# Kernel optimization log

Measured on AMD Instinct MI355X. Metric: run time of the kernel, lower is better.

The kernel has to match this reference:

```python
import jax, jax.numpy as jnp
from jax import lax
import numpy as np

THRESH = 0.5
R = 4  # suppression radius -> (2R+1)^3 max-pool window


def setup_inputs() -> dict:
    key = jax.random.key(0)
    pred_vol = jax.random.uniform(key, (1, 1, 64, 512, 512), dtype=jnp.float32)
    return {"pred_vol": pred_vol}


def reference(pred_vol):
    # Threshold: keep values above thresh, zero otherwise
    pred_thresh = jnp.where(pred_vol > THRESH, pred_vol, jnp.float32(0.0))
    # 3D max-pool, kernel 2R+1, stride 1, padding R (pad with -inf so padding
    k = 2 * R + 1
    conf = lax.reduce_window(
        pred_thresh,
        -jnp.inf,
        lax.max,
        window_dimensions=(1, 1, k, k, k),
        window_strides=(1, 1, 1, 1, 1),
        padding=[(0, 0), (0, 0), (R, R), (R, R), (R, R)],
    )
    # Keep only strict local maxima of the thresholded volume
    conf = jnp.where((conf > 0.0) & (conf == pred_thresh), conf, jnp.float32(0.0))
    return jnp.squeeze(conf)  # [D, H, W]
```

## Files before the change

### kernel.cpp

```cpp
#include <hip/hip_runtime.h>

static constexpr int Dd = 64;
static constexpr int Hh = 512;
static constexpr int Ww = 512;
static constexpr int RAD = 4;
static constexpr float THRESH_V = 0.5f;
static constexpr int W4 = Ww / 4;
static constexpr int PLANE4 = Hh * W4;

static constexpr int TH = 8;
static constexpr int DC = 16;
static constexpr int ROWS = TH + 2 * RAD;
static constexpr int NPL = DC + 2 * RAD;
static constexpr int NBLK = (Hh / TH) * (Dd / DC);

typedef float nf4 __attribute__((ext_vector_type(4)));

__device__ __forceinline__ float4 f4max(float4 a, float4 b) {
    return make_float4(fmaxf(a.x, b.x), fmaxf(a.y, b.y), fmaxf(a.z, b.z), fmaxf(a.w, b.w));
}
__device__ __forceinline__ int iclamp(int v, int lo, int hi) {
    return v < lo ? lo : (v > hi ? hi : v);
}

#define BAR_VM(N) asm volatile("s_waitcnt vmcnt(" #N ") lgkmcnt(0)\n\ts_barrier" ::: "memory")
#define BAR_LDS() asm volatile("s_waitcnt lgkmcnt(0)\n\ts_barrier" ::: "memory")

__device__ __forceinline__ void load_lds16(const float4* g, float4* l) {
    __builtin_amdgcn_global_load_lds(
        (const __attribute__((address_space(1))) void*)g,
        (__attribute__((address_space(3))) void*)l, 16, 0, 0);
}

__global__ __launch_bounds__(512, 1)
void fused_nms_k6(const float4* __restrict__ x4, float4* __restrict__ o4) {
    __shared__ float4 braw[3][ROWS * W4];
    __shared__ float4 bcol[TH * W4];

    const int tid  = threadIdx.x;
    const int w4   = tid & (W4 - 1);
    const int hs   = tid >> 7;
    const int wid  = tid >> 6;
    const int lane = tid & 63;

    const int b    = blockIdx.x;
    const int band = b & 7;
    const int rest = b >> 3;
    const int ht   = band * 8 + (rest & 7);
    const int dc   = rest >> 3;
    const int h0   = ht * TH;
    const int d0   = dc * DC;

    const int colm = w4 ? w4 - 1 : 0;
    const int colp = (w4 < W4 - 1) ? w4 + 1 : W4 - 1;

    int goff[4], loff[4];
#pragma unroll
    for (int k = 0; k < 4; ++k) {
        const int s    = wid + 8 * k;
        const int row  = s >> 1;
        const int half = s & 1;
        const int gh   = iclamp(h0 - RAD + row, 0, Hh - 1);
        goff[k] = gh * W4 + half * 64 + lane;
        loff[k] = row * W4 + half * 64;
    }

    auto stage = [&](int p) {
        const int gd = iclamp(d0 - RAD + p, 0, Dd - 1);
        const float4* pl = x4 + (size_t)gd * PLANE4;
        float4* dst = braw[p % 3];
#pragma unroll
        for (int k = 0; k < 4; ++k)
            load_lds16(pl + goff[k], dst + loff[k]);
    };

    auto hwin = [&](const float4 lm, const float4 cm, const float4 rm) -> float4 {
        const float l3 = lm.w, l2 = fmaxf(lm.z, l3), l1 = fmaxf(lm.y, l2), l0 = fmaxf(lm.x, l1);
        const float core = fmaxf(fmaxf(cm.x, cm.y), fmaxf(cm.z, cm.w));
        const float q0 = rm.x, q1 = fmaxf(q0, rm.y), q2 = fmaxf(q1, rm.z), q3 = fmaxf(q2, rm.w);
        float4 pm;
        pm.x = fmaxf(l0, fmaxf(core, q0));
        pm.y = fmaxf(l1, fmaxf(core, q1));
        pm.z = fmaxf(l2, fmaxf(core, q2));
        pm.w = fmaxf(l3, fmaxf(core, q3));
        return pm;
    };

    float4 R0[8], R1[8];
    float4 C0[4], C1[4];

    stage(0);
    stage(1);

#pragma unroll
    for (int t = 0; t < NPL; ++t) {
        const bool doE = (t >= 8);

        if (t <= 8)       { BAR_VM(4); }
        else if (t == 9)  { BAR_VM(6); }
        else if (t <= 22) { BAR_VM(8); }
        else              { BAR_VM(4); }

        if (t + 2 < NPL) stage(t + 2);
        __builtin_amdgcn_sched_barrier(0);

        const float4* Bc = &braw[t % 3][(2 * hs) * W4 + w4];
        float4 r0 = Bc[0 * W4], r1 = Bc[1 * W4], r2 = Bc[2 * W4], r3 = Bc[3 * W4];
        float4 r4 = Bc[4 * W4], r5 = Bc[5 * W4], r6 = Bc[6 * W4], r7 = Bc[7 * W4];
        float4 r8 = Bc[8 * W4], r9 = Bc[9 * W4];
        float4 core = f4max(f4max(f4max(r1, r2), f4max(r3, r4)),
                            f4max(f4max(r5, r6), f4max(r7, r8)));
        float4 v0 = f4max(core, r0);
        float4 v1 = f4max(core, r9);
        bcol[(2 * hs) * W4 + w4]     = v0;
        bcol[(2 * hs + 1) * W4 + w4] = v1;
        BAR_LDS();

        const float4 pm0 = hwin(bcol[(2 * hs) * W4 + colm],     v0, bcol[(2 * hs) * W4 + colp]);
        const float4 pm1 = hwin(bcol[(2 * hs + 1) * W4 + colm], v1, bcol[(2 * hs + 1) * W4 + colp]);

        if (doE) {
            const float4 cen0 = C0[t & 3];
            const float4 cen1 = C1[t & 3];
            float4 mm0 = pm0, mm1 = pm1;
#pragma unroll
            for (int i = 0; i < 8; ++i) { mm0 = f4max(mm0, R0[i]); mm1 = f4max(mm1, R1[i]); }
            const size_t obase = (size_t)(d0 + t - 8) * PLANE4 + (size_t)(h0 + 2 * hs) * W4 + w4;
            nf4 q0, q1;
            q0.x = (cen0.x > THRESH_V && cen0.x == mm0.x) ? cen0.x : 0.0f;
            q0.y = (cen0.y > THRESH_V && cen0.y == mm0.y) ? cen0.y : 0.0f;
            q0.z = (cen0.z > THRESH_V && cen0.z == mm0.z) ? cen0.z : 0.0f;
            q0.w = (cen0.w > THRESH_V && cen0.w == mm0.w) ? cen0.w : 0.0f;
            q1.x = (cen1.x > THRESH_V && cen1.x == mm1.x) ? cen1.x : 0.0f;
            q1.y = (cen1.y > THRESH_V && cen1.y == mm1.y) ? cen1.y : 0.0f;
            q1.z = (cen1.z > THRESH_V && cen1.z == mm1.z) ? cen1.z : 0.0f;
            q1.w = (cen1.w > THRESH_V && cen1.w == mm1.w) ? cen1.w : 0.0f;
            __builtin_nontemporal_store(q0, (nf4*)&o4[obase]);
            __builtin_nontemporal_store(q1, (nf4*)&o4[obase + W4]);
        }
        R0[t & 7] = pm0;  R1[t & 7] = pm1;
        C0[t & 3] = r4;   C1[t & 3] = r5;
    }
}

extern "C" void kernel_launch(void* const* d_in, const int* in_sizes, int n_in,
                              void* d_out, int out_size, void* d_ws, size_t ws_size,
                              hipStream_t stream) {
    const float4* x4 = (const float4*)d_in[0];
    float4* out4 = (float4*)d_out;
    (void)d_ws; (void)ws_size; (void)in_sizes; (void)n_in; (void)out_size;
    fused_nms_k6<<<dim3(NBLK), dim3(512), 0, stream>>>(x4, out4);
}
```

Before: 118.9 us.

## Software-pipeline vertical and horizontal max passes with double-buffered LDS

Double-buffers the column-max LDS buffer and skews the loop by one iteration, so the horizontal window for plane t-1 is computed in the same iteration as the vertical max for plane t. This removes one LDS barrier per plane between writing bcol and reading neighbours. The cost is one extra loop iteration, a larger center-value ring (5 entries), more registers and more LDS.

```diff
diff --git a/kernel.cpp b/kernel.cpp
--- a/kernel.cpp
+++ b/kernel.cpp
@@ -33,9 +33,9 @@
 }
 
 __global__ __launch_bounds__(512, 1)
-void fused_nms_k6(const float4* __restrict__ x4, float4* __restrict__ o4) {
+void fused_nms_k7(const float4* __restrict__ x4, float4* __restrict__ o4) {
     __shared__ float4 braw[3][ROWS * W4];
-    __shared__ float4 bcol[TH * W4];
+    __shared__ float4 bcol[2][TH * W4];
 
     const int tid  = threadIdx.x;
     const int w4   = tid & (W4 - 1);
@@ -87,59 +87,76 @@
     };
 
     float4 R0[8], R1[8];
-    float4 C0[4], C1[4];
+    float4 C0[5], C1[5];
+    float4 vp0, vp1;
 
     stage(0);
     stage(1);
 
 #pragma unroll
-    for (int t = 0; t < NPL; ++t) {
-        const bool doE = (t >= 8);
+    for (int t = 0; t <= NPL; ++t) {
+        const bool doV = (t <= NPL - 1);
+        const bool doH = (t >= 1);
+        const bool doE = (t >= 9);
 
-        if (t <= 8)       { BAR_VM(4); }
-        else if (t == 9)  { BAR_VM(6); }
+        if (t <= 9)       { BAR_VM(4); }
+        else if (t == 10) { BAR_VM(6); }
         else if (t <= 22) { BAR_VM(8); }
-        else              { BAR_VM(4); }
+        else if (t == 23) { BAR_VM(4); }
+        else              { BAR_LDS(); }
 
-        if (t + 2 < NPL) stage(t + 2);
+        if (t + 2 <= NPL - 1) stage(t + 2);
         __builtin_amdgcn_sched_barrier(0);
 
-        const float4* Bc = &braw[t % 3][(2 * hs) * W4 + w4];
-        float4 r0 = Bc[0 * W4], r1 = Bc[1 * W4], r2 = Bc[2 * W4], r3 = Bc[3 * W4];
-        float4 r4 = Bc[4 * W4], r5 = Bc[5 * W4], r6 = Bc[6 * W4], r7 = Bc[7 * W4];
-        float4 r8 = Bc[8 * W4], r9 = Bc[9 * W4];
-        float4 core = f4max(f4max(f4max(r1, r2), f4max(r3, r4)),
-                            f4max(f4max(r5, r6), f4max(r7, r8)));
-        float4 v0 = f4max(core, r0);
-        float4 v1 = f4max(core, r9);
-        bcol[(2 * hs) * W4 + w4]     = v0;
-        bcol[(2 * hs + 1) * W4 + w4] = v1;
-        BAR_LDS();
+        float4 nv0, nv1, nc0, nc1;
+        if (doV) {
+            const float4* Bc = &braw[t % 3][(2 * hs) * W4 + w4];
+            float4 r0 = Bc[0 * W4], r1 = Bc[1 * W4], r2 = Bc[2 * W4], r3 = Bc[3 * W4];
+            float4 r4 = Bc[4 * W4], r5 = Bc[5 * W4], r6 = Bc[6 * W4], r7 = Bc[7 * W4];
+            float4 r8 = Bc[8 * W4], r9 = Bc[9 * W4];
+            float4 core = f4max(f4max(f4max(r1, r2), f4max(r3, r4)),
+                                f4max(f4max(r5, r6), f4max(r7, r8)));
+            nv0 = f4max(core, r0);
+            nv1 = f4max(core, r9);
+            bcol[t & 1][(2 * hs) * W4 + w4]     = nv0;
+            bcol[t & 1][(2 * hs + 1) * W4 + w4] = nv1;
+            nc0 = r4;
+            nc1 = r5;
+        }
 
-        const float4 pm0 = hwin(bcol[(2 * hs) * W4 + colm],     v0, bcol[(2 * hs) * W4 + colp]);
-        const float4 pm1 = hwin(bcol[(2 * hs + 1) * W4 + colm], v1, bcol[(2 * hs + 1) * W4 + colp]);
+        if (doH) {
+            const float4* Bp = &bcol[(t - 1) & 1][0];
+            const float4 pm0 = hwin(Bp[(2 * hs) * W4 + colm],     vp0, Bp[(2 * hs) * W4 + colp]);
+            const float4 pm1 = hwin(Bp[(2 * hs + 1) * W4 + colm], vp1, Bp[(2 * hs + 1) * W4 + colp]);
 
-        if (doE) {
-            const float4 cen0 = C0[t & 3];
-            const float4 cen1 = C1[t & 3];
-            float4 mm0 = pm0, mm1 = pm1;
+            if (doE) {
+                const float4 cen0 = C0[t % 5];
+                const float4 cen1 = C1[t % 5];
+                float4 mm0 = pm0, mm1 = pm1;
 #pragma unroll
-            for (int i = 0; i < 8; ++i) { mm0 = f4max(mm0, R0[i]); mm1 = f4max(mm1, R1[i]); }
-            const size_t obase = (size_t)(d0 + t - 8) * PLANE4 + (size_t)(h0 + 2 * hs) * W4 + w4;
-            nf4 q0, q1;
-            q0.x = (cen0.x > THRESH_V && cen0.x == mm0.x) ? cen0.x : 0.0f;
-            q0.y = (cen0.y > THRESH_V && cen0.y == mm0.y) ? cen0.y : 0.0f;
-            q0.z = (cen0.z > THRESH_V && cen0.z == mm0.z) ? cen0.z : 0.0f;
-            q0.w = (cen0.w > THRESH_V && cen0.w == mm0.w) ? cen0.w : 0.0f;
-            q1.x = (cen1.x > THRESH_V && cen1.x == mm1.x) ? cen1.x : 0.0f;
-            q1.y = (cen1.y > THRESH_V && cen1.y == mm1.y) ? cen1.y : 0.0f;
-            q1.z = (cen1.z > THRESH_V && cen1.z == mm1.z) ? cen1.z : 0.0f;
-            q1.w = (cen1.w > THRESH_V && cen1.w == mm1.w) ? cen1.w : 0.0f;
-            __builtin_nontemporal_store(q0, (nf4*)&o4[obase]);
-            __builtin_nontemporal_store(q1, (nf4*)&o4[obase + W4]);
+                for (int i = 0; i < 8; ++i) { mm0 = f4max(mm0, R0[i]); mm1 = f4max(mm1, R1[i]); }
+                const size_t obase = (size_t)(d0 + t - 9) * PLANE4
+                                   + (size_t)(h0 + 2 * hs) * W4 + w4;
+                nf4 q0, q1;
+                q0.x = (cen0.x > THRESH_V && cen0.x == mm0.x) ? cen0.x : 0.0f;
+                q0.y = (cen0.y > THRESH_V && cen0.y == mm0.y) ? cen0.y : 0.0f;
+                q0.z = (cen0.z > THRESH_V && cen0.z == mm0.z) ? cen0.z : 0.0f;
+                q0.w = (cen0.w > THRESH_V && cen0.w == mm0.w) ? cen0.w : 0.0f;
+                q1.x = (cen1.x > THRESH_V && cen1.x == mm1.x) ? cen1.x : 0.0f;
+                q1.y = (cen1.y > THRESH_V && cen1.y == mm1.y) ? cen1.y : 0.0f;
+                q1.z = (cen1.z > THRESH_V && cen1.z == mm1.z) ? cen1.z : 0.0f;
+                q1.w = (cen1.w > THRESH_V && cen1.w == mm1.w) ? cen1.w : 0.0f;
+                __builtin_nontemporal_store(q0, (nf4*)&o4[obase]);
+                __builtin_nontemporal_store(q1, (nf4*)&o4[obase + W4]);
+            }
+            R0[(t - 1) & 7] = pm0;
+            R1[(t - 1) & 7] = pm1;
         }
-        R0[t & 7] = pm0;  R1[t & 7] = pm1;
-        C0[t & 3] = r4;   C1[t & 3] = r5;
+
+        if (doV) {
+            vp0 = nv0;  vp1 = nv1;
+            C0[t % 5] = nc0;  C1[t % 5] = nc1;
+        }
     }
 }
 
@@ -149,5 +166,5 @@
     const float4* x4 = (const float4*)d_in[0];
     float4* out4 = (float4*)d_out;
     (void)d_ws; (void)ws_size; (void)in_sizes; (void)n_in; (void)out_size;
-    fused_nms_k6<<<dim3(NBLK), dim3(512), 0, stream>>>(x4, out4);
+    fused_nms_k7<<<dim3(NBLK), dim3(512), 0, stream>>>(x4, out4);
 }
```

After: 116.1 us. 1.02x faster.
